# Performance work log

Measured on AMD Instinct MI355X. Metric: run time of the kernel, lower is better.

## Reference

```python
import jax, jax.numpy as jnp
import numpy as np

M = 255   # filter_order
P = 80    # frame_period


def setup_inputs() -> dict:
    key = jax.random.key(0)
    k1, k2 = jax.random.split(key)
    B, N = 8, 800
    T = N * P
    x = jax.random.normal(k1, (B, T), dtype=jnp.float32)
    h = jax.random.normal(k2, (B, N, M + 1), dtype=jnp.float32)
    return {"x": x, "h": h}


def _zerodf(x, h):
    # x: (B, T) excitation; h: (B, N, M+1) per-frame FIR coefficients, T = N*P
    B, T = x.shape
    N = h.shape[1]
    # left-pad with M zeros, then sliding windows of length M+1, stride 1
    x_pad = jnp.pad(x, ((0, 0), (M, 0)))                       # (B, T+M)
    idx = jnp.arange(T)[:, None] + jnp.arange(M + 1)[None, :]  # (T, M+1)
    xw = x_pad[:, idx]                                         # (B, T, M+1); window t = [x[t-M], ..., x[t]]
    # flip coeffs so xw . h_flip = sum_m h_m[t] * x[t-m]
    hf = h[..., ::-1]                                          # (B, N, M+1)
    # linear interpolation of coeffs from frame rate to sample rate,
    # holding the last frame (replicate pad): w[n*P+k] = lerp(h[n], h[n+1], k/P)
    hp = jnp.concatenate([hf, hf[:, -1:, :]], axis=1)          # (B, N+1, M+1)
    frac = (jnp.arange(P, dtype=x.dtype) / P)[None, None, :, None]  # (1,1,P,1)
    hi = hp[:, :-1, None, :] * (1.0 - frac) + hp[:, 1:, None, :] * frac  # (B,N,P,M+1)
    hi = hi.reshape(B, N * P, M + 1)                           # (B, T, M+1)
    return jnp.sum(xw * hi, axis=-1)                           # (B, T)


def reference(x, h):
    return _zerodf(x, h)
```

## Files before the change

### kernel.cpp

```cpp
#include <hip/hip_runtime.h>


#define TAPS 256
#define PP 80
#define BB 8
#define NN 800
#define TT (NN * PP)
#define FPB 16
#define TPF 20
#define RR 4
#define NTHREADS (FPB * TPF)
#define HSTRIDE 260
#define XB 260
#define XLEN (FPB * PP + XB + 4)
#define CHUNKS (NN / FPB)

__global__ __launch_bounds__(NTHREADS) void azdf_kernel(
    const float* __restrict__ x, const float* __restrict__ h,
    float* __restrict__ out)
{
    __shared__ float sh[(FPB + 1) * HSTRIDE];
    __shared__ float sx[XLEN];

    const int tid = threadIdx.x;
    const int blk = blockIdx.x;
    const int b   = blk / CHUNKS;
    const int nc  = blk % CHUNKS;
    const int n0  = nc * FPB;
    const int t0  = n0 * PP;

    const float* hb = h + (size_t)b * NN * TAPS;
    for (int i = tid; i < (FPB + 1) * (TAPS / 4); i += NTHREADS) {
        int r  = i >> 6;
        int q  = i & 63;
        int gr = n0 + r;
        if (gr > NN - 1) gr = NN - 1;
        float4 v = ((const float4*)(hb + (size_t)gr * TAPS))[q];
        ((float4*)(sh + r * HSTRIDE))[q] = v;
    }

    const float* xb = x + (size_t)b * TT;
    for (int i = tid; i < XLEN; i += NTHREADS) {
        int g = t0 + i - XB;
        sx[i] = (g >= 0 && g < TT) ? xb[g] : 0.0f;
    }
    __syncthreads();

    const int lf    = tid / TPF;
    const int p0    = (tid % TPF) * RR;
    const int xbase = XB + 4 * tid;
    const float* hA = sh + lf * HSTRIDE;
    const float* hB = hA + HSTRIDE;

    float acc0[RR], acc1[RR];
    #pragma unroll
    for (int r = 0; r < RR; ++r) { acc0[r] = 0.0f; acc1[r] = 0.0f; }

    float W[8];
    *(float4*)&W[0] = *(const float4*)&sx[xbase - 4];
    *(float4*)&W[4] = *(const float4*)&sx[xbase];

    float4 c0 = *(const float4*)hA;
    float4 c1 = *(const float4*)hB;

    #pragma unroll 4
    for (int k = 0; k < TAPS; k += 4) {
        float4 u0 = c0, u1 = c1;
        c0 = *(const float4*)(hA + k + 4);
        c1 = *(const float4*)(hB + k + 4);
        float4 xn = *(const float4*)&sx[xbase - k - 8];

        const float* u0f = (const float*)&u0;
        const float* u1f = (const float*)&u1;
        #pragma unroll
        for (int d = 0; d < 4; ++d) {
            float cc0 = u0f[d];
            float cc1 = u1f[d];
            #pragma unroll
            for (int r = 0; r < RR; ++r) {
                float xr = W[r - d + 4];
                acc0[r] = fmaf(xr, cc0, acc0[r]);
                acc1[r] = fmaf(xr, cc1, acc1[r]);
            }
        }
        W[4] = W[0]; W[5] = W[1]; W[6] = W[2]; W[7] = W[3];
        *(float4*)&W[0] = xn;
    }

    float4 o;
    float* of = (float*)&o;
    #pragma unroll
    for (int r = 0; r < RR; ++r) {
        float f = (float)(p0 + r) * (1.0f / PP);
        of[r] = acc0[r] + f * (acc1[r] - acc0[r]);
    }
    *(float4*)(out + (size_t)b * TT + t0 + 4 * tid) = o;
}

extern "C" void kernel_launch(void* const* d_in, const int* in_sizes, int n_in,
                              void* d_out, int out_size, void* d_ws, size_t ws_size,
                              hipStream_t stream) {
    const float* x = (const float*)d_in[0];
    const float* h = (const float*)d_in[1];
    float* out    = (float*)d_out;
    azdf_kernel<<<BB * CHUNKS, NTHREADS, 0, stream>>>(x, h, out);
}
```

Before: 74.02 us.

## Split filter taps across blocks and add a reduction kernel

Partitions the 256-tap FIR across four grid slices so each block accumulates only a quarter of the taps, writing partial outputs to a workspace. A second kernel sums the four partials into the output. This raises the block count and cuts per-block shared memory to improve occupancy and load balance across CUs. The cost is extra global traffic for the partials and a second kernel launch.

```diff
diff --git a/kernel.cpp b/kernel.cpp
--- a/kernel.cpp
+++ b/kernel.cpp
@@ -6,42 +6,49 @@
 #define BB 8
 #define NN 800
 #define TT (NN * PP)
+#define SPLITS 4
+#define KSPL (TAPS / SPLITS)
 #define FPB 16
 #define TPF 20
 #define RR 4
 #define NTHREADS (FPB * TPF)
-#define HSTRIDE 260
-#define XB 260
+#define HSTRIDE 68
+#define XB 68
 #define XLEN (FPB * PP + XB + 4)
 #define CHUNKS (NN / FPB)
 
-__global__ __launch_bounds__(NTHREADS) void azdf_kernel(
+__global__ __launch_bounds__(NTHREADS) void azdf_split_kernel(
     const float* __restrict__ x, const float* __restrict__ h,
-    float* __restrict__ out)
+    float* __restrict__ ws)
 {
     __shared__ float sh[(FPB + 1) * HSTRIDE];
     __shared__ float sx[XLEN];
 
-    const int tid = threadIdx.x;
-    const int blk = blockIdx.x;
-    const int b   = blk / CHUNKS;
-    const int nc  = blk % CHUNKS;
-    const int n0  = nc * FPB;
-    const int t0  = n0 * PP;
+    const int tid   = threadIdx.x;
+    const int blk   = blockIdx.x;
+    const int split = blockIdx.y;
+    const int ks    = split * KSPL;
+    const int b     = blk / CHUNKS;
+    const int nc    = blk % CHUNKS;
+    const int n0    = nc * FPB;
+    const int t0    = n0 * PP;
 
-    const float* hb = h + (size_t)b * NN * TAPS;
-    for (int i = tid; i < (FPB + 1) * (TAPS / 4); i += NTHREADS) {
-        int r  = i >> 6;
-        int q  = i & 63;
+    const float* hb = h + (size_t)b * NN * TAPS + ks;
+    for (int i = tid; i < (FPB + 1) * (KSPL / 4); i += NTHREADS) {
+        int r  = i >> 4;
+        int q  = i & 15;
         int gr = n0 + r;
         if (gr > NN - 1) gr = NN - 1;
         float4 v = ((const float4*)(hb + (size_t)gr * TAPS))[q];
         ((float4*)(sh + r * HSTRIDE))[q] = v;
     }
+    for (int r = tid; r < FPB + 1; r += NTHREADS) {
+        ((float4*)(sh + r * HSTRIDE))[KSPL / 4] = make_float4(0.f, 0.f, 0.f, 0.f);
+    }
 
     const float* xb = x + (size_t)b * TT;
     for (int i = tid; i < XLEN; i += NTHREADS) {
-        int g = t0 + i - XB;
+        int g = t0 - ks - XB + i;
         sx[i] = (g >= 0 && g < TT) ? xb[g] : 0.0f;
     }
     __syncthreads();
@@ -64,11 +71,11 @@
     float4 c1 = *(const float4*)hB;
 
     #pragma unroll 4
-    for (int k = 0; k < TAPS; k += 4) {
+    for (int kk = 0; kk < KSPL; kk += 4) {
         float4 u0 = c0, u1 = c1;
-        c0 = *(const float4*)(hA + k + 4);
-        c1 = *(const float4*)(hB + k + 4);
-        float4 xn = *(const float4*)&sx[xbase - k - 8];
+        c0 = *(const float4*)(hA + kk + 4);
+        c1 = *(const float4*)(hB + kk + 4);
+        float4 xn = *(const float4*)&sx[xbase - kk - 8];
 
         const float* u0f = (const float*)&u0;
         const float* u1f = (const float*)&u1;
@@ -94,7 +101,24 @@
         float f = (float)(p0 + r) * (1.0f / PP);
         of[r] = acc0[r] + f * (acc1[r] - acc0[r]);
     }
-    *(float4*)(out + (size_t)b * TT + t0 + 4 * tid) = o;
+    *(float4*)(ws + (size_t)split * BB * TT + (size_t)b * TT + t0 + 4 * tid) = o;
+}
+
+__global__ __launch_bounds__(256) void azdf_reduce_kernel(
+    const float* __restrict__ ws, float* __restrict__ out)
+{
+    int i = (blockIdx.x * 256 + threadIdx.x);
+    const float4* p0 = (const float4*)ws;
+    const float4* p1 = (const float4*)(ws + (size_t)1 * BB * TT);
+    const float4* p2 = (const float4*)(ws + (size_t)2 * BB * TT);
+    const float4* p3 = (const float4*)(ws + (size_t)3 * BB * TT);
+    float4 a = p0[i], b = p1[i], c = p2[i], d = p3[i];
+    float4 o;
+    o.x = (a.x + b.x) + (c.x + d.x);
+    o.y = (a.y + b.y) + (c.y + d.y);
+    o.z = (a.z + b.z) + (c.z + d.z);
+    o.w = (a.w + b.w) + (c.w + d.w);
+    ((float4*)out)[i] = o;
 }
 
 extern "C" void kernel_launch(void* const* d_in, const int* in_sizes, int n_in,
@@ -103,5 +127,11 @@
     const float* x = (const float*)d_in[0];
     const float* h = (const float*)d_in[1];
     float* out    = (float*)d_out;
-    azdf_kernel<<<BB * CHUNKS, NTHREADS, 0, stream>>>(x, h, out);
+    float* ws     = (float*)d_ws;
+
+    dim3 grid(BB * CHUNKS, SPLITS);
+    azdf_split_kernel<<<grid, NTHREADS, 0, stream>>>(x, h, ws);
+
+    int n4 = BB * TT / 4;
+    azdf_reduce_kernel<<<n4 / 256, 256, 0, stream>>>(ws, out);
 }
```

Result: no change. 74.87 us (+1.1%).
